# Kernel tuning notes

Measured on AMD Instinct MI355X. Metric: run time of the kernel, lower is better.

The kernel has to match this reference:

```python
import jax, jax.numpy as jnp
import numpy as np

PERI_IDX = np.array([0, 1, 2, 3, 5, 6, 7, 8])  # non-center taps of the 3x3 window


def _extract_patches(x, stride, padding):
    # x: [B,C,H,W] -> patches [B,C,9,Hout,Wout], tap k = di*3+dj (row-major), matching F.unfold.
    B, C, H, W = x.shape
    Hout = (H + 2 * padding - 3) // stride + 1
    Wout = (W + 2 * padding - 3) // stride + 1
    xp = jnp.pad(x, ((0, 0), (0, 0), (padding, padding), (padding, padding)))
    taps = [xp[:, :, di:di + (Hout - 1) * stride + 1:stride, dj:dj + (Wout - 1) * stride + 1:stride]
            for di in range(3) for dj in range(3)]
    return jnp.stack(taps, axis=2)  # [B,C,9,Hout,Wout]


def setup_inputs() -> dict:
    key = jax.random.key(0)
    k1, k2, k3, k4 = jax.random.split(key, 4)
    B, C, O, H, W = 8, 64, 64, 128, 128
    x = jax.random.normal(k1, (B, C, H, W), dtype=jnp.float32)
    core = jax.random.normal(k2, (O, C, 1, 1), dtype=jnp.float32) * (1.0 / np.sqrt(C))
    periphery = jax.random.uniform(k3, (8,), dtype=jnp.float32, minval=-0.1, maxval=0.1)
    threshold = jnp.array([0.1], dtype=jnp.float32)
    scale = jnp.array([10.0], dtype=jnp.float32)
    return {"x": x, "core": core, "periphery": periphery, "threshold": threshold,
            "scale": scale, "stride": 1, "padding": 1}


def reference(x, core, periphery, threshold, scale, stride, padding):
    B, C, H, W = x.shape
    O = core.shape[0]
    patches = _extract_patches(x, stride, padding)           # [B,C,9,Ho,Wo]
    center = patches[:, :, 4]                                 # [B,C,Ho,Wo]
    # per-pixel variance-like routing statistic over channels and taps
    div = jnp.sum((patches - center[:, :, None]) ** 2, axis=(1, 2))  # [B,Ho,Wo]
    m_hard = jax.nn.sigmoid((div - threshold[0]) * scale[0]) > 0.5   # [B,Ho,Wo] bool
    w = core.reshape(O, C)
    # path 0 (low variance): 1x1 conv on the center pixel
    zero_out = jnp.einsum('bchw,oc->bohw', center, w)
    # path 1 (high variance): periphery-weighted sum then 1x1 conv
    agg = jnp.einsum('bckhw,k->bchw', patches[:, :, PERI_IDX], periphery)
    one_out = jnp.einsum('bchw,oc->bohw', agg, w)
    return jnp.where(m_hard[:, None], one_out, zero_out)
```

## Files before the change

kernel.cpp:

```cpp
#include <hip/hip_runtime.h>
#include <hip/hip_bf16.h>

constexpr int Bc = 8;
constexpr int Cc = 64;
constexpr int Oc = 64;
constexpr int Hc = 128;
constexpr int Wc = 128;
constexpr int HWc = Hc * Wc;
constexpr int CP = 72;

typedef __attribute__((ext_vector_type(8))) short short8;
typedef __attribute__((ext_vector_type(4))) float floatx4;

__global__ __launch_bounds__(512, 4) void spconv_kernel(
    const float* __restrict__ x, const float* __restrict__ core,
    const float* __restrict__ peri, const float* __restrict__ thr,
    const float* __restrict__ scl, float* __restrict__ out)
{
    __shared__ __hip_bfloat16 s_selT[2][Wc][CP];
    __shared__ __hip_bfloat16 s_core[Oc][CP];
    __shared__ float s_divp[2][4][Wc];
    __shared__ float s_msk[2][Wc];
    __shared__ int   s_any;

    const int tid = threadIdx.x;
    const int w   = tid & (Wc - 1);
    const int q   = tid >> 7;
    const int b   = blockIdx.x & 7;
    const int hp  = blockIdx.x >> 3;
    const int h0  = hp * 2;

    if (tid == 0) s_any = 0;

    #pragma unroll
    for (int i = 0; i < 8; ++i) {
        const int idx = i * 512 + tid;
        s_core[idx >> 6][idx & 63] = __float2bfloat16(core[idx]);
    }

    const float* xb = x + (size_t)b * Cc * HWc + (size_t)h0 * Wc;

    const float mU  = (h0 > 0) ? 1.f : 0.f;
    const float mD2 = (h0 < Hc - 2) ? 1.f : 0.f;
    const int   dU  = (h0 > 0) ? -Wc : 0;
    const int   dD2 = (h0 < Hc - 2) ? 2 * Wc : Wc;
    const float mL = (w > 0) ? 1.f : 0.f;
    const float mR = (w < Wc - 1) ? 1.f : 0.f;
    const int   oL = (w > 0) ? w - 1 : w;
    const int   oR = (w < Wc - 1) ? w + 1 : w;
    const float mUL = mU * mL,  mUR = mU * mR;
    const float mDL = mD2 * mL, mDR = mD2 * mR;

    const float p0 = peri[0], p1 = peri[1], p2 = peri[2], p3 = peri[3];
    const float p4 = peri[4], p5 = peri[5], p6 = peri[6], p7 = peri[7];

    float dvA = 0.f, dvB = 0.f;
    const float* rowq = xb + (size_t)(q * 16) * HWc;
    #pragma unroll 4
    for (int ci = 0; ci < 16; ++ci) {
        const float* r0 = rowq + (size_t)ci * HWc;
        const float* rm = r0 + dU;
        const float* r1 = r0 + Wc;
        const float* r2 = r0 + dD2;

        float ul = rm[oL], uc = rm[w], ur = rm[oR];
        float cl = r0[oL], cc = r0[w], cr = r0[oR];
        float dl = r1[oL], dc = r1[w], dr = r1[oR];
        float el = r2[oL], ec = r2[w], er = r2[oR];

        ul *= mUL; uc *= mU;  ur *= mUR;
        const float clm = cl * mL, crm = cr * mR;
        const float dlm = dl * mL, drm = dr * mR;
        el *= mDL; ec *= mD2; er *= mDR;

        float aggA =     p0 * ul;
        aggA = fmaf(p1, uc,  aggA);
        aggA = fmaf(p2, ur,  aggA);
        aggA = fmaf(p3, clm, aggA);
        aggA = fmaf(p4, crm, aggA);
        aggA = fmaf(p5, dlm, aggA);
        aggA = fmaf(p6, dc,  aggA);
        aggA = fmaf(p7, drm, aggA);
        s_selT[0][w][q * 16 + ci] = __float2bfloat16(aggA);

        float e_;
        e_ = ul  - cc; dvA = fmaf(e_, e_, dvA);
        e_ = uc  - cc; dvA = fmaf(e_, e_, dvA);
        e_ = ur  - cc; dvA = fmaf(e_, e_, dvA);
        e_ = clm - cc; dvA = fmaf(e_, e_, dvA);
        e_ = crm - cc; dvA = fmaf(e_, e_, dvA);
        e_ = dlm - cc; dvA = fmaf(e_, e_, dvA);
        e_ = dc  - cc; dvA = fmaf(e_, e_, dvA);
        e_ = drm - cc; dvA = fmaf(e_, e_, dvA);

        float aggB =     p0 * clm;
        aggB = fmaf(p1, cc,  aggB);
        aggB = fmaf(p2, crm, aggB);
        aggB = fmaf(p3, dlm, aggB);
        aggB = fmaf(p4, drm, aggB);
        aggB = fmaf(p5, el,  aggB);
        aggB = fmaf(p6, ec,  aggB);
        aggB = fmaf(p7, er,  aggB);
        s_selT[1][w][q * 16 + ci] = __float2bfloat16(aggB);

        e_ = clm - dc; dvB = fmaf(e_, e_, dvB);
        e_ = cc  - dc; dvB = fmaf(e_, e_, dvB);
        e_ = crm - dc; dvB = fmaf(e_, e_, dvB);
        e_ = dlm - dc; dvB = fmaf(e_, e_, dvB);
        e_ = drm - dc; dvB = fmaf(e_, e_, dvB);
        e_ = el  - dc; dvB = fmaf(e_, e_, dvB);
        e_ = ec  - dc; dvB = fmaf(e_, e_, dvB);
        e_ = er  - dc; dvB = fmaf(e_, e_, dvB);
    }
    s_divp[0][q][w] = dvA;
    s_divp[1][q][w] = dvB;
    __syncthreads();

    const int lane = tid & 63;
    const int wid  = tid >> 6;
    const int o0   = (wid & 3) * 16;
    const int wh   = wid >> 2;
    const int n    = lane & 15;
    const int quad = lane >> 4;
    const short8 a0 = *(const short8*)&s_core[o0 + n][quad * 8];
    const short8 a1 = *(const short8*)&s_core[o0 + n][quad * 8 + 32];

    if (tid < 2 * Wc) {
        const int rr = tid >> 7, ww = tid & (Wc - 1);
        const float div = s_divp[rr][0][ww] + s_divp[rr][1][ww]
                        + s_divp[rr][2][ww] + s_divp[rr][3][ww];
        const bool one = ((div - thr[0]) * scl[0]) > 0.f;
        s_msk[rr][ww] = one ? 1.f : 0.f;
        if (!one) s_any = 1;
    }
    __syncthreads();

    if (s_any) {
        #pragma unroll
        for (int i = 0; i < 32; ++i) {
            const int idx = i * 512 + tid;
            const int rr  = idx >> 13;
            const int e2  = idx & 8191;
            const int ww  = e2 & (Wc - 1);
            const int c   = e2 >> 7;
            if (s_msk[rr][ww] == 0.f)
                s_selT[rr][ww][c] =
                    __float2bfloat16(xb[(size_t)c * HWc + rr * Wc + ww]);
        }
        __syncthreads();
    }

    float* outb = out + ((size_t)(b * Oc) * Hc + h0) * Wc;

    #pragma unroll
    for (int rr = 0; rr < 2; ++rr) {
        #pragma unroll
        for (int t = 0; t < 4; ++t) {
            const int w0 = (wh * 4 + t) * 16;
            const short8 b0 = *(const short8*)&s_selT[rr][w0 + n][quad * 8];
            const short8 b1 = *(const short8*)&s_selT[rr][w0 + n][quad * 8 + 32];
            floatx4 acc = {0.f, 0.f, 0.f, 0.f};
            acc = __builtin_amdgcn_mfma_f32_16x16x32_bf16(a0, b0, acc, 0, 0, 0);
            acc = __builtin_amdgcn_mfma_f32_16x16x32_bf16(a1, b1, acc, 0, 0, 0);
            #pragma unroll
            for (int r = 0; r < 4; ++r) {
                const int o = o0 + quad * 4 + r;
                outb[(size_t)o * HWc + rr * Wc + w0 + n] = acc[r];
            }
        }
    }
}

extern "C" void kernel_launch(void* const* d_in, const int* in_sizes, int n_in,
                              void* d_out, int out_size, void* d_ws, size_t ws_size,
                              hipStream_t stream) {
    const float* x    = (const float*)d_in[0];
    const float* core = (const float*)d_in[1];
    const float* peri = (const float*)d_in[2];
    const float* thr  = (const float*)d_in[3];
    const float* scl  = (const float*)d_in[4];
    float* out = (float*)d_out;

    spconv_kernel<<<dim3(Bc * Hc / 2), dim3(512), 0, stream>>>(
        x, core, peri, thr, scl, out);
}
```

Before: 100.5 us.

## Load two pixels per lane with float2 and share neighbors via ds_bpermute

The stencil phase is reorganised so each lane of a wavefront owns two adjacent columns and loads them as float2. Left and right neighbours come from cross-lane ds_bpermute instead of extra global loads, and each wave handles 8 channels, so the partial divergence sums grow to 8 slices. The bf16 transpose buffer uses a permuted column order, with index remapping in the fallback fill and the MFMA B-operand loads. Packed bf16 conversion instructions are also used for the weights and activations. This cuts redundant global loads and conversion instructions, at the cost of bpermute LDS traffic and more complex indexing.

```diff
diff --git a/kernel.cpp b/kernel.cpp
--- a/kernel.cpp
+++ b/kernel.cpp
@@ -11,6 +11,16 @@
 
 typedef __attribute__((ext_vector_type(8))) short short8;
 typedef __attribute__((ext_vector_type(4))) float floatx4;
+typedef __attribute__((ext_vector_type(2))) float floatx2;
+
+__device__ __forceinline__ float bperm(int idx4, float v) {
+    return __int_as_float(__builtin_amdgcn_ds_bpermute(idx4, __float_as_int(v)));
+}
+__device__ __forceinline__ unsigned cvt_pk_bf16(float lo, float hi) {
+    unsigned r;
+    asm("v_cvt_pk_bf16_f32 %0, %1, %2" : "=v"(r) : "v"(lo), "v"(hi));
+    return r;
+}
 
 __global__ __launch_bounds__(512, 4) void spconv_kernel(
     const float* __restrict__ x, const float* __restrict__ core,
@@ -19,13 +29,13 @@
 {
     __shared__ __hip_bfloat16 s_selT[2][Wc][CP];
     __shared__ __hip_bfloat16 s_core[Oc][CP];
-    __shared__ float s_divp[2][4][Wc];
+    __shared__ float s_divp[2][8][Wc];
     __shared__ float s_msk[2][Wc];
     __shared__ int   s_any;
 
     const int tid = threadIdx.x;
-    const int w   = tid & (Wc - 1);
-    const int q   = tid >> 7;
+    const int l   = tid & 63;
+    const int wv  = tid >> 6;
     const int b   = blockIdx.x & 7;
     const int hp  = blockIdx.x >> 3;
     const int h0  = hp * 2;
@@ -33,103 +43,125 @@
     if (tid == 0) s_any = 0;
 
     #pragma unroll
-    for (int i = 0; i < 8; ++i) {
-        const int idx = i * 512 + tid;
-        s_core[idx >> 6][idx & 63] = __float2bfloat16(core[idx]);
-    }
-
-    const float* xb = x + (size_t)b * Cc * HWc + (size_t)h0 * Wc;
-
-    const float mU  = (h0 > 0) ? 1.f : 0.f;
-    const float mD2 = (h0 < Hc - 2) ? 1.f : 0.f;
+    for (int i = 0; i < 2; ++i) {
+        const int idx = (i * 512 + tid) * 4;
+        const floatx4 v = *(const floatx4*)(core + idx);
+        unsigned* dst = (unsigned*)&s_core[idx >> 6][idx & 63];
+        dst[0] = cvt_pk_bf16(v.x, v.y);
+        dst[1] = cvt_pk_bf16(v.z, v.w);
+    }
+
+    const int upIdx = ((l - 1) & 63) << 2;
+    const int dnIdx = ((l + 1) & 63) << 2;
+    const float lzf = (l == 0)  ? 0.f : 1.f;
+    const float rzf = (l == 63) ? 0.f : 1.f;
+    const float mUf = (h0 > 0) ? 1.f : 0.f;
+    const float mDf = (h0 < Hc - 2) ? 1.f : 0.f;
     const int   dU  = (h0 > 0) ? -Wc : 0;
     const int   dD2 = (h0 < Hc - 2) ? 2 * Wc : Wc;
-    const float mL = (w > 0) ? 1.f : 0.f;
-    const float mR = (w < Wc - 1) ? 1.f : 0.f;
-    const int   oL = (w > 0) ? w - 1 : w;
-    const int   oR = (w < Wc - 1) ? w + 1 : w;
-    const float mUL = mU * mL,  mUR = mU * mR;
-    const float mDL = mD2 * mL, mDR = mD2 * mR;
 
     const float p0 = peri[0], p1 = peri[1], p2 = peri[2], p3 = peri[3];
     const float p4 = peri[4], p5 = peri[5], p6 = peri[6], p7 = peri[7];
 
-    float dvA = 0.f, dvB = 0.f;
-    const float* rowq = xb + (size_t)(q * 16) * HWc;
-    #pragma unroll 4
-    for (int ci = 0; ci < 16; ++ci) {
-        const float* r0 = rowq + (size_t)ci * HWc;
-        const float* rm = r0 + dU;
-        const float* r1 = r0 + Wc;
-        const float* r2 = r0 + dD2;
-
-        float ul = rm[oL], uc = rm[w], ur = rm[oR];
-        float cl = r0[oL], cc = r0[w], cr = r0[oR];
-        float dl = r1[oL], dc = r1[w], dr = r1[oR];
-        float el = r2[oL], ec = r2[w], er = r2[oR];
-
-        ul *= mUL; uc *= mU;  ur *= mUR;
-        const float clm = cl * mL, crm = cr * mR;
-        const float dlm = dl * mL, drm = dr * mR;
-        el *= mDL; ec *= mD2; er *= mDR;
-
-        float aggA =     p0 * ul;
-        aggA = fmaf(p1, uc,  aggA);
-        aggA = fmaf(p2, ur,  aggA);
-        aggA = fmaf(p3, clm, aggA);
-        aggA = fmaf(p4, crm, aggA);
-        aggA = fmaf(p5, dlm, aggA);
-        aggA = fmaf(p6, dc,  aggA);
-        aggA = fmaf(p7, drm, aggA);
-        s_selT[0][w][q * 16 + ci] = __float2bfloat16(aggA);
-
-        float e_;
-        e_ = ul  - cc; dvA = fmaf(e_, e_, dvA);
-        e_ = uc  - cc; dvA = fmaf(e_, e_, dvA);
-        e_ = ur  - cc; dvA = fmaf(e_, e_, dvA);
-        e_ = clm - cc; dvA = fmaf(e_, e_, dvA);
-        e_ = crm - cc; dvA = fmaf(e_, e_, dvA);
-        e_ = dlm - cc; dvA = fmaf(e_, e_, dvA);
-        e_ = dc  - cc; dvA = fmaf(e_, e_, dvA);
-        e_ = drm - cc; dvA = fmaf(e_, e_, dvA);
-
-        float aggB =     p0 * clm;
-        aggB = fmaf(p1, cc,  aggB);
-        aggB = fmaf(p2, crm, aggB);
-        aggB = fmaf(p3, dlm, aggB);
-        aggB = fmaf(p4, drm, aggB);
-        aggB = fmaf(p5, el,  aggB);
-        aggB = fmaf(p6, ec,  aggB);
-        aggB = fmaf(p7, er,  aggB);
-        s_selT[1][w][q * 16 + ci] = __float2bfloat16(aggB);
-
-        e_ = clm - dc; dvB = fmaf(e_, e_, dvB);
-        e_ = cc  - dc; dvB = fmaf(e_, e_, dvB);
-        e_ = crm - dc; dvB = fmaf(e_, e_, dvB);
-        e_ = dlm - dc; dvB = fmaf(e_, e_, dvB);
-        e_ = drm - dc; dvB = fmaf(e_, e_, dvB);
-        e_ = el  - dc; dvB = fmaf(e_, e_, dvB);
-        e_ = ec  - dc; dvB = fmaf(e_, e_, dvB);
-        e_ = er  - dc; dvB = fmaf(e_, e_, dvB);
-    }
-    s_divp[0][q][w] = dvA;
-    s_divp[1][q][w] = dvB;
+    const float* xw = x + (size_t)b * Cc * HWc + (size_t)h0 * Wc + 2 * l;
+    const float* xb = x + (size_t)b * Cc * HWc + (size_t)h0 * Wc;
+
+    float dAlo = 0.f, dAhi = 0.f, dBlo = 0.f, dBhi = 0.f;
+
+#define PROC(RM, R0, R1, R2, K) do {                                          \
+    const float rmL = lzf * bperm(upIdx, RM.y);                               \
+    const float r0L = lzf * bperm(upIdx, R0.y);                               \
+    const float r1L = lzf * bperm(upIdx, R1.y);                               \
+    const float r2L = lzf * bperm(upIdx, R2.y);                               \
+    const float rmR = rzf * bperm(dnIdx, RM.x);                               \
+    const float r0R = rzf * bperm(dnIdx, R0.x);                               \
+    const float r1R = rzf * bperm(dnIdx, R1.x);                               \
+    const float r2R = rzf * bperm(dnIdx, R2.x);                               \
+    { const float t = R0.x;                       \
+      float a = p0 * rmL; a = fmaf(p1, RM.x, a); a = fmaf(p2, RM.y, a);       \
+      a = fmaf(p3, r0L, a); a = fmaf(p4, R0.y, a);                            \
+      a = fmaf(p5, r1L, a); a = fmaf(p6, R1.x, a); a = fmaf(p7, R1.y, a);     \
+      aAlo[K] = a; float e;                                                   \
+      e = rmL  - t; dAlo = fmaf(e, e, dAlo); e = RM.x - t; dAlo = fmaf(e, e, dAlo); \
+      e = RM.y - t; dAlo = fmaf(e, e, dAlo); e = r0L  - t; dAlo = fmaf(e, e, dAlo); \
+      e = R0.y - t; dAlo = fmaf(e, e, dAlo); e = r1L  - t; dAlo = fmaf(e, e, dAlo); \
+      e = R1.x - t; dAlo = fmaf(e, e, dAlo); e = R1.y - t; dAlo = fmaf(e, e, dAlo); } \
+    { const float t = R0.y;                     \
+      float a = p0 * RM.x; a = fmaf(p1, RM.y, a); a = fmaf(p2, rmR, a);       \
+      a = fmaf(p3, R0.x, a); a = fmaf(p4, r0R, a);                            \
+      a = fmaf(p5, R1.x, a); a = fmaf(p6, R1.y, a); a = fmaf(p7, r1R, a);     \
+      aAhi[K] = a; float e;                                                   \
+      e = RM.x - t; dAhi = fmaf(e, e, dAhi); e = RM.y - t; dAhi = fmaf(e, e, dAhi); \
+      e = rmR  - t; dAhi = fmaf(e, e, dAhi); e = R0.x - t; dAhi = fmaf(e, e, dAhi); \
+      e = r0R  - t; dAhi = fmaf(e, e, dAhi); e = R1.x - t; dAhi = fmaf(e, e, dAhi); \
+      e = R1.y - t; dAhi = fmaf(e, e, dAhi); e = r1R  - t; dAhi = fmaf(e, e, dAhi); } \
+    { const float t = R1.x;                              \
+      float a = p0 * r0L; a = fmaf(p1, R0.x, a); a = fmaf(p2, R0.y, a);       \
+      a = fmaf(p3, r1L, a); a = fmaf(p4, R1.y, a);                            \
+      a = fmaf(p5, r2L, a); a = fmaf(p6, R2.x, a); a = fmaf(p7, R2.y, a);     \
+      aBlo[K] = a; float e;                                                   \
+      e = r0L  - t; dBlo = fmaf(e, e, dBlo); e = R0.x - t; dBlo = fmaf(e, e, dBlo); \
+      e = R0.y - t; dBlo = fmaf(e, e, dBlo); e = r1L  - t; dBlo = fmaf(e, e, dBlo); \
+      e = R1.y - t; dBlo = fmaf(e, e, dBlo); e = r2L  - t; dBlo = fmaf(e, e, dBlo); \
+      e = R2.x - t; dBlo = fmaf(e, e, dBlo); e = R2.y - t; dBlo = fmaf(e, e, dBlo); } \
+    { const float t = R1.y;                              \
+      float a = p0 * R0.x; a = fmaf(p1, R0.y, a); a = fmaf(p2, r0R, a);       \
+      a = fmaf(p3, R1.x, a); a = fmaf(p4, r1R, a);                            \
+      a = fmaf(p5, R2.x, a); a = fmaf(p6, R2.y, a); a = fmaf(p7, r2R, a);     \
+      aBhi[K] = a; float e;                                                   \
+      e = R0.x - t; dBhi = fmaf(e, e, dBhi); e = R0.y - t; dBhi = fmaf(e, e, dBhi); \
+      e = r0R  - t; dBhi = fmaf(e, e, dBhi); e = R1.x - t; dBhi = fmaf(e, e, dBhi); \
+      e = r1R  - t; dBhi = fmaf(e, e, dBhi); e = R2.x - t; dBhi = fmaf(e, e, dBhi); \
+      e = R2.y - t; dBhi = fmaf(e, e, dBhi); e = r2R  - t; dBhi = fmaf(e, e, dBhi); } \
+} while (0)
+
+    #pragma unroll 2
+    for (int j = 0; j < 4; ++j) {
+        const int c0 = wv * 8 + 2 * j;
+        const float* b0p = xw + (size_t)c0 * HWc;
+        const float* b1p = b0p + HWc;
+
+        floatx2 rm0 = *(const floatx2*)(b0p + dU);
+        floatx2 r00 = *(const floatx2*)(b0p);
+        floatx2 r10 = *(const floatx2*)(b0p + Wc);
+        floatx2 r20 = *(const floatx2*)(b0p + dD2);
+        floatx2 rm1 = *(const floatx2*)(b1p + dU);
+        floatx2 r01 = *(const floatx2*)(b1p);
+        floatx2 r11 = *(const floatx2*)(b1p + Wc);
+        floatx2 r21 = *(const floatx2*)(b1p + dD2);
+        rm0 *= mUf; r20 *= mDf; rm1 *= mUf; r21 *= mDf;
+
+        float aAlo[2], aAhi[2], aBlo[2], aBhi[2];
+        PROC(rm0, r00, r10, r20, 0);
+        PROC(rm1, r01, r11, r21, 1);
+
+        *(unsigned*)&s_selT[0][l]      [c0] = cvt_pk_bf16(aAlo[0], aAlo[1]);
+        *(unsigned*)&s_selT[0][64 + l] [c0] = cvt_pk_bf16(aAhi[0], aAhi[1]);
+        *(unsigned*)&s_selT[1][l]      [c0] = cvt_pk_bf16(aBlo[0], aBlo[1]);
+        *(unsigned*)&s_selT[1][64 + l] [c0] = cvt_pk_bf16(aBhi[0], aBhi[1]);
+    }
+#undef PROC
+
+    {
+        floatx2 da = {dAlo, dAhi}, db = {dBlo, dBhi};
+        *(floatx2*)&s_divp[0][wv][2 * l] = da;
+        *(floatx2*)&s_divp[1][wv][2 * l] = db;
+    }
     __syncthreads();
 
-    const int lane = tid & 63;
-    const int wid  = tid >> 6;
-    const int o0   = (wid & 3) * 16;
-    const int wh   = wid >> 2;
-    const int n    = lane & 15;
-    const int quad = lane >> 4;
+    const int o0   = (wv & 3) * 16;
+    const int wh   = wv >> 2;
+    const int n    = l & 15;
+    const int quad = l >> 4;
     const short8 a0 = *(const short8*)&s_core[o0 + n][quad * 8];
     const short8 a1 = *(const short8*)&s_core[o0 + n][quad * 8 + 32];
 
     if (tid < 2 * Wc) {
         const int rr = tid >> 7, ww = tid & (Wc - 1);
-        const float div = s_divp[rr][0][ww] + s_divp[rr][1][ww]
-                        + s_divp[rr][2][ww] + s_divp[rr][3][ww];
-        const bool one = ((div - thr[0]) * scl[0]) > 0.f;
+        float dv = s_divp[rr][0][ww];
+        #pragma unroll
+        for (int g = 1; g < 8; ++g) dv += s_divp[rr][g][ww];
+        const bool one = ((dv - thr[0]) * scl[0]) > 0.f;
         s_msk[rr][ww] = one ? 1.f : 0.f;
         if (!one) s_any = 1;
     }
@@ -141,10 +173,11 @@
             const int idx = i * 512 + tid;
             const int rr  = idx >> 13;
             const int e2  = idx & 8191;
-            const int ww  = e2 & (Wc - 1);
+            const int p   = e2 & (Wc - 1);
             const int c   = e2 >> 7;
+            const int ww  = ((p & 63) << 1) | (p >> 6);
             if (s_msk[rr][ww] == 0.f)
-                s_selT[rr][ww][c] =
+                s_selT[rr][p][c] =
                     __float2bfloat16(xb[(size_t)c * HWc + rr * Wc + ww]);
         }
         __syncthreads();
@@ -156,9 +189,11 @@
     for (int rr = 0; rr < 2; ++rr) {
         #pragma unroll
         for (int t = 0; t < 4; ++t) {
-            const int w0 = (wh * 4 + t) * 16;
-            const short8 b0 = *(const short8*)&s_selT[rr][w0 + n][quad * 8];
-            const short8 b1 = *(const short8*)&s_selT[rr][w0 + n][quad * 8 + 32];
+            const int w0   = (wh * 4 + t) * 16;
+            const int wlog = w0 + n;
+            const int pr   = ((wlog >> 1) & 63) | ((wlog & 1) << 6);
+            const short8 b0 = *(const short8*)&s_selT[rr][pr][quad * 8];
+            const short8 b1 = *(const short8*)&s_selT[rr][pr][quad * 8 + 32];
             floatx4 acc = {0.f, 0.f, 0.f, 0.f};
             acc = __builtin_amdgcn_mfma_f32_16x16x32_bf16(a0, b0, acc, 0, 0, 0);
             acc = __builtin_amdgcn_mfma_f32_16x16x32_bf16(a1, b1, acc, 0, 0, 0);
```

Result: faster. 97.39 us, median of 2 (-3.1%).
